# Performance work log

Measured on AMD Instinct MI355X. Metric: run time of the kernel, lower is better.

## Reference

```python
import jax, jax.numpy as jnp
import numpy as np

SEQ = 2048
HID = 4096
N_HEADS = 32
N_KV = 8
HEAD_DIM = 128
EPS = 1e-6


def _rope_tables(max_pos, dim, base=10000.0):
    inv_freq = 1.0 / (base ** (np.arange(0, dim, 2, dtype=np.float32) / dim))
    t = np.arange(max_pos, dtype=np.float32)
    freqs = np.outer(t, inv_freq)                     # [P, D/2]
    emb = np.concatenate([freqs, freqs], axis=-1)     # [P, D]
    return jnp.asarray(np.cos(emb)), jnp.asarray(np.sin(emb))


def setup_inputs() -> dict:
    key = jax.random.key(0)
    ks = jax.random.split(key, 6)
    s = 0.02
    cos, sin = _rope_tables(SEQ, HEAD_DIM)
    causal = jnp.tril(jnp.ones((SEQ, SEQ), dtype=bool))
    attn_mask = jnp.where(causal, 0.0, -1e9).astype(jnp.float32)
    return {
        "x": jax.random.normal(ks[0], (SEQ, HID), dtype=jnp.float32),
        "position_ids": jnp.arange(SEQ, dtype=jnp.int32),
        "cos": cos,
        "sin": sin,
        "attn_mask": attn_mask,
        "Wq": jax.random.normal(ks[1], (HID, N_HEADS * HEAD_DIM), dtype=jnp.float32) * s,
        "Wk": jax.random.normal(ks[2], (HID, N_KV * HEAD_DIM), dtype=jnp.float32) * s,
        "Wv": jax.random.normal(ks[3], (HID, N_KV * HEAD_DIM), dtype=jnp.float32) * s,
        "Wo": jax.random.normal(ks[4], (N_HEADS * HEAD_DIM, HID), dtype=jnp.float32) * s,
        "q_norm_w": jnp.ones((HEAD_DIM,), dtype=jnp.float32),
        "k_norm_w": jnp.ones((HEAD_DIM,), dtype=jnp.float32),
    }


def _rms_norm(x, w):
    # x: [H, S, D]; normalize over last dim
    return w * (x * jax.lax.rsqrt(jnp.mean(x * x, axis=-1, keepdims=True) + EPS))


def _apply_rope(x, cos, sin, position_ids):
    # x: [H, S, D]; cos/sin: [P, D]
    c = cos[position_ids][None]  # [1, S, D]
    s = sin[position_ids][None]
    half = x.shape[-1] // 2
    x1, x2 = x[..., :half], x[..., half:]
    rotated = jnp.concatenate([-x2, x1], axis=-1)
    return x * c + rotated * s


def reference(x, position_ids, cos, sin, attn_mask, Wq, Wk, Wv, Wo, q_norm_w, k_norm_w):
    S = x.shape[0]
    q = (x @ Wq).reshape(S, N_HEADS, HEAD_DIM).transpose(1, 0, 2)   # [H, S, D]
    k = (x @ Wk).reshape(S, N_KV, HEAD_DIM).transpose(1, 0, 2)      # [Hkv, S, D]
    v = (x @ Wv).reshape(S, N_KV, HEAD_DIM).transpose(1, 0, 2)
    q = _rms_norm(q, q_norm_w)
    k = _rms_norm(k, k_norm_w)
    q = _apply_rope(q, cos, sin, position_ids)
    k = _apply_rope(k, cos, sin, position_ids)
    # GQA: repeat_interleave kv heads to match q heads
    groups = N_HEADS // N_KV
    k = jnp.repeat(k, groups, axis=0)  # [H, S, D]
    v = jnp.repeat(v, groups, axis=0)
    scores = jnp.einsum("hqd,hkd->hqk", q, k) * (HEAD_DIM ** -0.5)
    scores = scores + attn_mask  # broadcast [S,S] -> [H,S,S]
    attn = jax.nn.softmax(scores.astype(jnp.float32), axis=-1).astype(x.dtype)
    out = jnp.einsum("hqk,hkd->hqd", attn, v)   # [H, S, D]
    out = out.transpose(1, 0, 2).reshape(S, N_HEADS * HEAD_DIM)
    return out @ Wo
```

## Files before the change

### kernel.cpp

```cpp
#include <hip/hip_runtime.h>

typedef unsigned short u16;
typedef __attribute__((ext_vector_type(8))) short bf16x8;
typedef __attribute__((ext_vector_type(4))) float f32x4;

__device__ __forceinline__ float bf2f(u16 b) {
    unsigned int u = ((unsigned int)b) << 16;
    float f;
    __builtin_memcpy(&f, &u, 4);
    return f;
}
__device__ __forceinline__ u16 f2bf(float f) {
    unsigned int u;
    __builtin_memcpy(&u, &f, 4);
    unsigned int r = u + 0x7FFFu + ((u >> 16) & 1u);
    return (u16)(r >> 16);
}

__device__ __forceinline__ void async_copy16(const void* g, void* lds) {
    __builtin_amdgcn_global_load_lds(
        (const __attribute__((address_space(1))) unsigned int*)g,
        (__attribute__((address_space(3))) unsigned int*)lds, 16, 0, 0);
}

#define MFMA(a, b, c) __builtin_amdgcn_mfma_f32_16x16x32_bf16((a), (b), (c), 0, 0, 0)

__global__ __launch_bounds__(256) void cvt_f32_bf16(
    const float* __restrict__ src, u16* __restrict__ dst)
{
    int i = (blockIdx.x * 256 + threadIdx.x) * 8;
    float4 a = *(const float4*)(src + i);
    float4 b = *(const float4*)(src + i + 4);
    uint4 o;
    u16* po = (u16*)&o;
    po[0] = f2bf(a.x); po[1] = f2bf(a.y); po[2] = f2bf(a.z); po[3] = f2bf(a.w);
    po[4] = f2bf(b.x); po[5] = f2bf(b.y); po[6] = f2bf(b.z); po[7] = f2bf(b.w);
    *(uint4*)(dst + i) = o;
}

__global__ __launch_bounds__(256) void transpose_cvt(
    const float* __restrict__ src, u16* __restrict__ dst, int R, int C)
{
    __shared__ u16 T[64][65];
    int r0 = blockIdx.y * 64, c0 = blockIdx.x * 64;
    int t = threadIdx.x;
#pragma unroll
    for (int i = 0; i < 4; ++i) {
        int c = i * 256 + t;
        int row = c >> 4, col4 = (c & 15) * 4;
        float4 v = *(const float4*)(src + (size_t)(r0 + row) * C + c0 + col4);
        T[row][col4 + 0] = f2bf(v.x);
        T[row][col4 + 1] = f2bf(v.y);
        T[row][col4 + 2] = f2bf(v.z);
        T[row][col4 + 3] = f2bf(v.w);
    }
    __syncthreads();
#pragma unroll
    for (int i = 0; i < 2; ++i) {
        int c = i * 256 + t;
        int row = c >> 3, col8 = (c & 7) * 8;
        uint4 o;
        u16* po = (u16*)&o;
#pragma unroll
        for (int j = 0; j < 8; ++j) po[j] = T[col8 + j][row];
        *(uint4*)(dst + (size_t)(c0 + row) * R + r0 + col8) = o;
    }
}

template <bool F32OUT>
__global__ __launch_bounds__(256) void gemm_bt(
    const u16* __restrict__ A, const u16* __restrict__ Bt, void* __restrict__ Cp,
    int M, int N, int K)
{
    __shared__ u16 As[128][64];
    __shared__ u16 Bs[128][64];
    int tid = threadIdx.x;
    int w = tid >> 6, lane = tid & 63;
    int quad = lane >> 4, l15 = lane & 15;
    int m0 = blockIdx.y * 128, n0 = blockIdx.x * 128;
    int wm = w >> 1, wn = w & 1;

    f32x4 acc[4][4] = {};

    for (int k0 = 0; k0 < K; k0 += 64) {
#pragma unroll
        for (int i = 0; i < 4; ++i) {
            int row = w * 32 + i * 8 + (lane >> 3);
            int s = lane & 7;
            int gc = s ^ (row & 7);
            async_copy16(A + (size_t)(m0 + row) * K + k0 + gc * 8, &As[w * 32 + i * 8][0]);
            async_copy16(Bt + (size_t)(n0 + row) * K + k0 + gc * 8, &Bs[w * 32 + i * 8][0]);
        }
        __syncthreads();
#pragma unroll
        for (int kk = 0; kk < 2; ++kk) {
            bf16x8 a[4], b[4];
            int kq = kk * 4 + quad;
#pragma unroll
            for (int mt = 0; mt < 4; ++mt) {
                int m = wm * 64 + mt * 16 + l15;
                a[mt] = *(const bf16x8*)&As[m][(kq ^ (m & 7)) * 8];
            }
#pragma unroll
            for (int nt = 0; nt < 4; ++nt) {
                int n = wn * 64 + nt * 16 + l15;
                b[nt] = *(const bf16x8*)&Bs[n][(kq ^ (n & 7)) * 8];
            }
#pragma unroll
            for (int mt = 0; mt < 4; ++mt)
#pragma unroll
                for (int nt = 0; nt < 4; ++nt)
                    acc[mt][nt] = MFMA(a[mt], b[nt], acc[mt][nt]);
        }
        __syncthreads();
    }

#pragma unroll
    for (int mt = 0; mt < 4; ++mt)
#pragma unroll
        for (int nt = 0; nt < 4; ++nt)
#pragma unroll
            for (int r = 0; r < 4; ++r) {
                int m = m0 + wm * 64 + mt * 16 + quad * 4 + r;
                int n = n0 + wn * 64 + nt * 16 + l15;
                if (F32OUT)
                    ((float*)Cp)[(size_t)m * N + n] = acc[mt][nt][r];
                else
                    ((u16*)Cp)[(size_t)m * N + n] = f2bf(acc[mt][nt][r]);
            }
}

__global__ __launch_bounds__(256) void norm_rope(
    const u16* __restrict__ QKV, const int* __restrict__ pos,
    const float* __restrict__ cosT, const float* __restrict__ sinT,
    const float* __restrict__ qw, const float* __restrict__ kw,
    u16* __restrict__ Qr, u16* __restrict__ Kr)
{
    int gw = blockIdx.x * 4 + (threadIdx.x >> 6);
    int lane = threadIdx.x & 63;
    int s = gw / 40;
    int hh = gw - s * 40;
    bool isq = hh < 32;
    int h = isq ? hh : hh - 32;
    int col0 = isq ? h * 128 : 4096 + h * 128;
    const u16* x = QKV + (size_t)s * 6144 + col0;
    float x1 = bf2f(x[lane]);
    float x2 = bf2f(x[lane + 64]);
    float ss = x1 * x1 + x2 * x2;
#pragma unroll
    for (int m = 1; m < 64; m <<= 1) ss += __shfl_xor(ss, m);
    float r = rsqrtf(ss * (1.0f / 128.0f) + 1e-6f);
    const float* wgt = isq ? qw : kw;
    float y1 = x1 * r * wgt[lane];
    float y2 = x2 * r * wgt[lane + 64];
    int p = pos[s];
    float c1 = cosT[p * 128 + lane], c2 = cosT[p * 128 + lane + 64];
    float s1 = sinT[p * 128 + lane], s2 = sinT[p * 128 + lane + 64];
    float o1 = y1 * c1 - y2 * s1;
    float o2 = y2 * c2 + y1 * s2;
    u16* dst = (isq ? Qr : Kr) + ((size_t)h * 2048 + s) * 128;
    dst[lane] = f2bf(o1);
    dst[lane + 64] = f2bf(o2);
}

__global__ __launch_bounds__(256) void v_transpose(
    const u16* __restrict__ QKV, u16* __restrict__ Vt)
{
    __shared__ u16 T[64][130];
    int s0 = blockIdx.x * 64;
    int kh = blockIdx.y;
    int t = threadIdx.x;
#pragma unroll
    for (int i = 0; i < 4; ++i) {
        int c = i * 256 + t;
        int srow = c >> 4, d8 = (c & 15) * 8;
        uint4 v = *(const uint4*)(QKV + (size_t)(s0 + srow) * 6144 + 5120 + kh * 128 + d8);
        const u16* pv = (const u16*)&v;
#pragma unroll
        for (int j = 0; j < 8; ++j) T[srow][d8 + j] = pv[j];
    }
    __syncthreads();
#pragma unroll
    for (int i = 0; i < 4; ++i) {
        int c = i * 256 + t;
        int drow = c >> 3, s8 = (c & 7) * 8;
        uint4 o;
        u16* po = (u16*)&o;
#pragma unroll
        for (int j = 0; j < 8; ++j) po[j] = T[s8 + j][drow];
        *(uint4*)(Vt + ((size_t)kh * 128 + drow) * 2048 + s0 + s8) = o;
    }
}

__global__ __launch_bounds__(256, 2) void flash_attn2(
    const u16* __restrict__ Qr, const u16* __restrict__ Kr,
    const u16* __restrict__ Vt, u16* __restrict__ O)
{
    __shared__ u16 Ks[2][64][128];
    __shared__ u16 Vs[2][128][64];
    __shared__ u16 Ps[4][32][64];

    int f = blockIdx.x + 64 * blockIdx.y;
    int lo = f & 255, hi = f >> 8;
    int qt  = hi ? 63 - (lo & 63) : (lo & 63);
    int kvh = (lo >> 6) + hi * 4;

    int tid = threadIdx.x;
    int w = tid >> 6, lane = tid & 63;
    int quad = lane >> 4, l15 = lane & 15;
    int h = kvh * 4 + w;
    int q0 = qt * 32;
    int nkt = qt / 2 + 1;

    bf16x8 qf[2][4];
#pragma unroll
    for (int mt = 0; mt < 2; ++mt) {
        const u16* qb = Qr + ((size_t)h * 2048 + q0 + mt * 16 + l15) * 128;
#pragma unroll
        for (int kk = 0; kk < 4; ++kk)
            qf[mt][kk] = *(const bf16x8*)(qb + kk * 32 + quad * 8);
    }

    float m_i[8], l_i[8];
#pragma unroll
    for (int r = 0; r < 8; ++r) { m_i[r] = -__builtin_inff(); l_i[r] = 0.0f; }
    f32x4 acc[2][8] = {};

    const float scale = 0.08838834764831845f;
    const float L2E = 1.44269504f;

    auto stage = [&](int kt, int b) {
        int k0 = kt * 64;
#pragma unroll
        for (int i = 0; i < 4; ++i) {
            int idx = (w * 4 + i) * 64 + lane;
            int krow = idx >> 4, kp = idx & 15;
            int kg = (kp & 8) | ((kp ^ krow) & 7);
            async_copy16(Kr + ((size_t)kvh * 2048 + k0 + krow) * 128 + kg * 8,
                         &Ks[b][(w * 4 + i) * 4][0]);
            int vrow = idx >> 3, vp = idx & 7;
            int vg = vp ^ (vrow & 7);
            async_copy16(Vt + ((size_t)kvh * 128 + vrow) * 2048 + k0 + vg * 8,
                         &Vs[b][(w * 4 + i) * 8][0]);
        }
    };

    stage(0, 0);

    for (int kt = 0; kt < nkt; ++kt) {
        int b = kt & 1;
        int k0 = kt * 64;
        __syncthreads();
        if (kt + 1 < nkt) stage(kt + 1, b ^ 1);

        f32x4 sa[2][4] = {};
#pragma unroll
        for (int nt = 0; nt < 4; ++nt) {
            int krow = nt * 16 + l15;
#pragma unroll
            for (int kk = 0; kk < 4; ++kk) {
                int kq = kk * 4 + quad;
                int kph = (kq & 8) | ((kq ^ krow) & 7);
                bf16x8 kf = *(const bf16x8*)&Ks[b][krow][kph * 8];
                sa[0][nt] = MFMA(qf[0][kk], kf, sa[0][nt]);
                sa[1][nt] = MFMA(qf[1][kk], kf, sa[1][nt]);
            }
        }

        bool last = (kt == nkt - 1);
        float pv[2][4][4], mloc[8];
#pragma unroll
        for (int r = 0; r < 8; ++r) mloc[r] = -__builtin_inff();
#pragma unroll
        for (int mt = 0; mt < 2; ++mt)
#pragma unroll
            for (int nt = 0; nt < 4; ++nt)
#pragma unroll
                for (int r = 0; r < 4; ++r) {
                    float v = sa[mt][nt][r] * scale;
                    if (last) {
                        int key = k0 + nt * 16 + l15;
                        int qrow = q0 + mt * 16 + quad * 4 + r;
                        if (key > qrow) v = -__builtin_inff();
                    }
                    pv[mt][nt][r] = v;
                    mloc[mt * 4 + r] = fmaxf(mloc[mt * 4 + r], v);
                }
#pragma unroll
        for (int r = 0; r < 8; ++r)
#pragma unroll
            for (int m = 1; m < 16; m <<= 1)
                mloc[r] = fmaxf(mloc[r], __shfl_xor(mloc[r], m));

        float alpha[8];
#pragma unroll
        for (int mt = 0; mt < 2; ++mt)
#pragma unroll
            for (int r = 0; r < 4; ++r) {
                int rr = mt * 4 + r;
                float mnew = fmaxf(m_i[rr], mloc[rr]);
                alpha[rr] = exp2f((m_i[rr] - mnew) * L2E);
                m_i[rr] = mnew;
                float rs = 0.0f;
#pragma unroll
                for (int nt = 0; nt < 4; ++nt) {
                    float p = exp2f((pv[mt][nt][r] - mnew) * L2E);
                    pv[mt][nt][r] = p;
                    rs += p;
                }
#pragma unroll
                for (int m = 1; m < 16; m <<= 1) rs += __shfl_xor(rs, m);
                l_i[rr] = l_i[rr] * alpha[rr] + rs;
            }
#pragma unroll
        for (int mt = 0; mt < 2; ++mt)
#pragma unroll
            for (int nt = 0; nt < 8; ++nt)
#pragma unroll
                for (int r = 0; r < 4; ++r) acc[mt][nt][r] *= alpha[mt * 4 + r];

#pragma unroll
        for (int mt = 0; mt < 2; ++mt)
#pragma unroll
            for (int nt = 0; nt < 4; ++nt)
#pragma unroll
                for (int r = 0; r < 4; ++r) {
                    int row = mt * 16 + quad * 4 + r;
                    int col = nt * 16 + l15;
                    int ph = ((col >> 3) ^ (row & 7)) * 8 + (col & 7);
                    Ps[w][row][ph] = f2bf(pv[mt][nt][r]);
                }
        asm volatile("s_waitcnt lgkmcnt(0)" ::: "memory");

        bf16x8 pf[2][2];
#pragma unroll
        for (int mt = 0; mt < 2; ++mt) {
            int row = mt * 16 + l15;
#pragma unroll
            for (int kk = 0; kk < 2; ++kk)
                pf[mt][kk] = *(const bf16x8*)&Ps[w][row][((kk * 4 + quad) ^ (row & 7)) * 8];
        }

#pragma unroll
        for (int nt = 0; nt < 8; ++nt) {
            int vrow = nt * 16 + l15;
#pragma unroll
            for (int kk = 0; kk < 2; ++kk) {
                int vph = (kk * 4 + quad) ^ (vrow & 7);
                bf16x8 vf = *(const bf16x8*)&Vs[b][vrow][vph * 8];
                acc[0][nt] = MFMA(pf[0][kk], vf, acc[0][nt]);
                acc[1][nt] = MFMA(pf[1][kk], vf, acc[1][nt]);
            }
        }
    }

#pragma unroll
    for (int mt = 0; mt < 2; ++mt)
#pragma unroll
        for (int nt = 0; nt < 8; ++nt)
#pragma unroll
            for (int r = 0; r < 4; ++r) {
                int qrow = q0 + mt * 16 + quad * 4 + r;
                int d = nt * 16 + l15;
                O[(size_t)qrow * 4096 + h * 128 + d] =
                    f2bf(acc[mt][nt][r] / l_i[mt * 4 + r]);
            }
}

extern "C" void kernel_launch(void* const* d_in, const int* in_sizes, int n_in,
                              void* d_out, int out_size, void* d_ws, size_t ws_size,
                              hipStream_t stream) {
    const float* x    = (const float*)d_in[0];
    const int*   pos  = (const int*)d_in[1];
    const float* cosT = (const float*)d_in[2];
    const float* sinT = (const float*)d_in[3];
    const float* Wq = (const float*)d_in[5];
    const float* Wk = (const float*)d_in[6];
    const float* Wv = (const float*)d_in[7];
    const float* Wo = (const float*)d_in[8];
    const float* qw = (const float*)d_in[9];
    const float* kw = (const float*)d_in[10];
    float* out = (float*)d_out;

    char* ws = (char*)d_ws;
    u16* WT  = (u16*)ws;
    u16* QKV = (u16*)(ws + 50331648ull);
    u16* Qr  = (u16*)(ws + 75497472ull);
    u16* Kr  = (u16*)(ws + 92274688ull);
    u16* Vt  = (u16*)(ws + 96468992ull);
    u16* Xb  = (u16*)(ws + 100663296ull);
    u16* AttnOut = QKV;

    dim3 blk(256);
    cvt_f32_bf16<<<dim3(4096), blk, 0, stream>>>(x, Xb);
    transpose_cvt<<<dim3(64, 64), blk, 0, stream>>>(Wq, WT, 4096, 4096);
    transpose_cvt<<<dim3(16, 64), blk, 0, stream>>>(Wk, WT + 4096ull * 4096, 4096, 1024);
    transpose_cvt<<<dim3(16, 64), blk, 0, stream>>>(Wv, WT + 5120ull * 4096, 4096, 1024);
    gemm_bt<false><<<dim3(48, 16), blk, 0, stream>>>(Xb, WT, QKV, 2048, 6144, 4096);
    norm_rope<<<dim3(20480), blk, 0, stream>>>(QKV, pos, cosT, sinT, qw, kw, Qr, Kr);
    v_transpose<<<dim3(32, 8), blk, 0, stream>>>(QKV, Vt);
    transpose_cvt<<<dim3(64, 64), blk, 0, stream>>>(Wo, WT, 4096, 4096);
    flash_attn2<<<dim3(64, 8), blk, 0, stream>>>(Qr, Kr, Vt, AttnOut);
    gemm_bt<true><<<dim3(32, 16), blk, 0, stream>>>(AttnOut, WT, out, 2048, 4096, 4096);
}
```

Before: 552.4 us.

## Drop online-softmax max tracking, split long causal rows across blocks with atomics

```diff
diff --git a/kernel.cpp b/kernel.cpp
--- a/kernel.cpp
+++ b/kernel.cpp
@@ -13,8 +13,7 @@
 __device__ __forceinline__ u16 f2bf(float f) {
     unsigned int u;
     __builtin_memcpy(&u, &f, 4);
-    unsigned int r = u + 0x7FFFu + ((u >> 16) & 1u);
-    return (u16)(r >> 16);
+    return (u16)((u + 0x8000u) >> 16);
 }
 
 __device__ __forceinline__ void async_copy16(const void* g, void* lds) {
@@ -192,25 +191,38 @@
     }
 }
 
-__global__ __launch_bounds__(256, 2) void flash_attn2(
+__global__ __launch_bounds__(256, 3) void flash_attn3(
     const u16* __restrict__ Qr, const u16* __restrict__ Kr,
-    const u16* __restrict__ Vt, u16* __restrict__ O)
-{
-    __shared__ u16 Ks[2][64][128];
-    __shared__ u16 Vs[2][128][64];
+    const u16* __restrict__ Vt, u16* __restrict__ O,
+    float* __restrict__ Oacc, float* __restrict__ Lacc)
+{
+    __shared__ u16 Ks[64][128];
+    __shared__ u16 Vs[128][64];
     __shared__ u16 Ps[4][32][64];
 
-    int f = blockIdx.x + 64 * blockIdx.y;
-    int lo = f & 255, hi = f >> 8;
-    int qt  = hi ? 63 - (lo & 63) : (lo & 63);
-    int kvh = (lo >> 6) + hi * 4;
+    int f = blockIdx.x;
+    int kvh = f / 95;
+    int j = f - kvh * 95;
+    int qt, kt0, len;
+    bool split;
+    if (j < 33) {
+        qt = j; kt0 = 0; len = (qt >> 1) + 1; split = false;
+    } else {
+        int jj = j - 33;
+        qt = 33 + (jj >> 1);
+        int n = (qt >> 1) + 1;
+        int h1 = (n + 1) >> 1;
+        if (jj & 1) { kt0 = h1; len = n - h1; }
+        else        { kt0 = 0;  len = h1; }
+        split = true;
+    }
+    int ndiag = qt >> 1;
+    int q0 = qt * 32;
 
     int tid = threadIdx.x;
     int w = tid >> 6, lane = tid & 63;
     int quad = lane >> 4, l15 = lane & 15;
     int h = kvh * 4 + w;
-    int q0 = qt * 32;
-    int nkt = qt / 2 + 1;
 
     bf16x8 qf[2][4];
 #pragma unroll
@@ -221,37 +233,31 @@
             qf[mt][kk] = *(const bf16x8*)(qb + kk * 32 + quad * 8);
     }
 
-    float m_i[8], l_i[8];
-#pragma unroll
-    for (int r = 0; r < 8; ++r) { m_i[r] = -__builtin_inff(); l_i[r] = 0.0f; }
     f32x4 acc[2][8] = {};
-
-    const float scale = 0.08838834764831845f;
-    const float L2E = 1.44269504f;
-
-    auto stage = [&](int kt, int b) {
+    f32x4 accl[2] = {};
+    bf16x8 ones;
+#pragma unroll
+    for (int i = 0; i < 8; ++i) ones[i] = (short)0x3F80;
+
+    const float C = 0.08838834764831845f * 1.44269504f;
+
+    for (int it = 0; it < len; ++it) {
+        int kt = kt0 + it;
         int k0 = kt * 64;
+        __syncthreads();
 #pragma unroll
         for (int i = 0; i < 4; ++i) {
             int idx = (w * 4 + i) * 64 + lane;
             int krow = idx >> 4, kp = idx & 15;
             int kg = (kp & 8) | ((kp ^ krow) & 7);
             async_copy16(Kr + ((size_t)kvh * 2048 + k0 + krow) * 128 + kg * 8,
-                         &Ks[b][(w * 4 + i) * 4][0]);
+                         &Ks[(w * 4 + i) * 4][0]);
             int vrow = idx >> 3, vp = idx & 7;
             int vg = vp ^ (vrow & 7);
             async_copy16(Vt + ((size_t)kvh * 128 + vrow) * 2048 + k0 + vg * 8,
-                         &Vs[b][(w * 4 + i) * 8][0]);
-        }
-    };
-
-    stage(0, 0);
-
-    for (int kt = 0; kt < nkt; ++kt) {
-        int b = kt & 1;
-        int k0 = kt * 64;
+                         &Vs[(w * 4 + i) * 8][0]);
+        }
         __syncthreads();
-        if (kt + 1 < nkt) stage(kt + 1, b ^ 1);
 
         f32x4 sa[2][4] = {};
 #pragma unroll
@@ -261,74 +267,29 @@
             for (int kk = 0; kk < 4; ++kk) {
                 int kq = kk * 4 + quad;
                 int kph = (kq & 8) | ((kq ^ krow) & 7);
-                bf16x8 kf = *(const bf16x8*)&Ks[b][krow][kph * 8];
+                bf16x8 kf = *(const bf16x8*)&Ks[krow][kph * 8];
                 sa[0][nt] = MFMA(qf[0][kk], kf, sa[0][nt]);
                 sa[1][nt] = MFMA(qf[1][kk], kf, sa[1][nt]);
             }
         }
 
-        bool last = (kt == nkt - 1);
-        float pv[2][4][4], mloc[8];
-#pragma unroll
-        for (int r = 0; r < 8; ++r) mloc[r] = -__builtin_inff();
+        bool diag = (kt == ndiag);
 #pragma unroll
         for (int mt = 0; mt < 2; ++mt)
 #pragma unroll
             for (int nt = 0; nt < 4; ++nt)
 #pragma unroll
                 for (int r = 0; r < 4; ++r) {
-                    float v = sa[mt][nt][r] * scale;
-                    if (last) {
+                    float p = exp2f(sa[mt][nt][r] * C);
+                    if (diag) {
                         int key = k0 + nt * 16 + l15;
                         int qrow = q0 + mt * 16 + quad * 4 + r;
-                        if (key > qrow) v = -__builtin_inff();
+                        if (key > qrow) p = 0.0f;
                     }
-                    pv[mt][nt][r] = v;
-                    mloc[mt * 4 + r] = fmaxf(mloc[mt * 4 + r], v);
-                }
-#pragma unroll
-        for (int r = 0; r < 8; ++r)
-#pragma unroll
-            for (int m = 1; m < 16; m <<= 1)
-                mloc[r] = fmaxf(mloc[r], __shfl_xor(mloc[r], m));
-
-        float alpha[8];
-#pragma unroll
-        for (int mt = 0; mt < 2; ++mt)
-#pragma unroll
-            for (int r = 0; r < 4; ++r) {
-                int rr = mt * 4 + r;
-                float mnew = fmaxf(m_i[rr], mloc[rr]);
-                alpha[rr] = exp2f((m_i[rr] - mnew) * L2E);
-                m_i[rr] = mnew;
-                float rs = 0.0f;
-#pragma unroll
-                for (int nt = 0; nt < 4; ++nt) {
-                    float p = exp2f((pv[mt][nt][r] - mnew) * L2E);
-                    pv[mt][nt][r] = p;
-                    rs += p;
-                }
-#pragma unroll
-                for (int m = 1; m < 16; m <<= 1) rs += __shfl_xor(rs, m);
-                l_i[rr] = l_i[rr] * alpha[rr] + rs;
-            }
-#pragma unroll
-        for (int mt = 0; mt < 2; ++mt)
-#pragma unroll
-            for (int nt = 0; nt < 8; ++nt)
-#pragma unroll
-                for (int r = 0; r < 4; ++r) acc[mt][nt][r] *= alpha[mt * 4 + r];
-
-#pragma unroll
-        for (int mt = 0; mt < 2; ++mt)
-#pragma unroll
-            for (int nt = 0; nt < 4; ++nt)
-#pragma unroll
-                for (int r = 0; r < 4; ++r) {
                     int row = mt * 16 + quad * 4 + r;
                     int col = nt * 16 + l15;
                     int ph = ((col >> 3) ^ (row & 7)) * 8 + (col & 7);
-                    Ps[w][row][ph] = f2bf(pv[mt][nt][r]);
+                    Ps[w][row][ph] = f2bf(p);
                 }
         asm volatile("s_waitcnt lgkmcnt(0)" ::: "memory");
 
@@ -347,24 +308,63 @@
 #pragma unroll
             for (int kk = 0; kk < 2; ++kk) {
                 int vph = (kk * 4 + quad) ^ (vrow & 7);
-                bf16x8 vf = *(const bf16x8*)&Vs[b][vrow][vph * 8];
+                bf16x8 vf = *(const bf16x8*)&Vs[vrow][vph * 8];
                 acc[0][nt] = MFMA(pf[0][kk], vf, acc[0][nt]);
                 acc[1][nt] = MFMA(pf[1][kk], vf, acc[1][nt]);
             }
         }
-    }
-
-#pragma unroll
-    for (int mt = 0; mt < 2; ++mt)
-#pragma unroll
-        for (int nt = 0; nt < 8; ++nt)
-#pragma unroll
-            for (int r = 0; r < 4; ++r) {
-                int qrow = q0 + mt * 16 + quad * 4 + r;
-                int d = nt * 16 + l15;
-                O[(size_t)qrow * 4096 + h * 128 + d] =
-                    f2bf(acc[mt][nt][r] / l_i[mt * 4 + r]);
-            }
+#pragma unroll
+        for (int mt = 0; mt < 2; ++mt)
+#pragma unroll
+            for (int kk = 0; kk < 2; ++kk)
+                accl[mt] = MFMA(pf[mt][kk], ones, accl[mt]);
+    }
+
+    if (!split) {
+#pragma unroll
+        for (int mt = 0; mt < 2; ++mt)
+#pragma unroll
+            for (int nt = 0; nt < 8; ++nt)
+#pragma unroll
+                for (int r = 0; r < 4; ++r) {
+                    int qrow = q0 + mt * 16 + quad * 4 + r;
+                    int d = nt * 16 + l15;
+                    O[(size_t)qrow * 4096 + h * 128 + d] =
+                        f2bf(acc[mt][nt][r] / accl[mt][r]);
+                }
+    } else {
+        int base = q0 - 1056;
+#pragma unroll
+        for (int mt = 0; mt < 2; ++mt)
+#pragma unroll
+            for (int nt = 0; nt < 8; ++nt)
+#pragma unroll
+                for (int r = 0; r < 4; ++r) {
+                    int row = base + mt * 16 + quad * 4 + r;
+                    int d = nt * 16 + l15;
+                    atomicAdd(&Oacc[((size_t)h * 992 + row) * 128 + d], acc[mt][nt][r]);
+                }
+        if (l15 == 0) {
+#pragma unroll
+            for (int mt = 0; mt < 2; ++mt)
+#pragma unroll
+                for (int r = 0; r < 4; ++r)
+                    atomicAdd(&Lacc[h * 992 + base + mt * 16 + quad * 4 + r],
+                              accl[mt][r]);
+        }
+    }
+}
+
+__global__ __launch_bounds__(256) void normalize_split(
+    const float* __restrict__ Oacc, const float* __restrict__ Lacc,
+    u16* __restrict__ O)
+{
+    int e = blockIdx.x * 256 + threadIdx.x;
+    int hd = e / 126976;
+    int rem = e - hd * 126976;
+    int row = rem >> 7, d = rem & 127;
+    float v = Oacc[e] / Lacc[hd * 992 + row];
+    O[(size_t)(1056 + row) * 4096 + hd * 128 + d] = f2bf(v);
 }
 
 extern "C" void kernel_launch(void* const* d_in, const int* in_sizes, int n_in,
@@ -390,6 +390,8 @@
     u16* Vt  = (u16*)(ws + 96468992ull);
     u16* Xb  = (u16*)(ws + 100663296ull);
     u16* AttnOut = QKV;
+    float* Oacc = (float*)Xb;
+    float* Lacc = (float*)((char*)Xb + 16252928ull);
 
     dim3 blk(256);
     cvt_f32_bf16<<<dim3(4096), blk, 0, stream>>>(x, Xb);
@@ -397,9 +399,11 @@
     transpose_cvt<<<dim3(16, 64), blk, 0, stream>>>(Wk, WT + 4096ull * 4096, 4096, 1024);
     transpose_cvt<<<dim3(16, 64), blk, 0, stream>>>(Wv, WT + 5120ull * 4096, 4096, 1024);
     gemm_bt<false><<<dim3(48, 16), blk, 0, stream>>>(Xb, WT, QKV, 2048, 6144, 4096);
+    hipMemsetAsync(Oacc, 0, 16379904ull, stream);
     norm_rope<<<dim3(20480), blk, 0, stream>>>(QKV, pos, cosT, sinT, qw, kw, Qr, Kr);
     v_transpose<<<dim3(32, 8), blk, 0, stream>>>(QKV, Vt);
     transpose_cvt<<<dim3(64, 64), blk, 0, stream>>>(Wo, WT, 4096, 4096);
-    flash_attn2<<<dim3(64, 8), blk, 0, stream>>>(Qr, Kr, Vt, AttnOut);
+    flash_attn3<<<dim3(760), blk, 0, stream>>>(Qr, Kr, Vt, AttnOut, Oacc, Lacc);
+    normalize_split<<<dim3(15872), blk, 0, stream>>>(Oacc, Lacc, AttnOut);
     gemm_bt<true><<<dim3(32, 16), blk, 0, stream>>>(AttnOut, WT, out, 2048, 4096, 4096);
 }
```

Result: slower. 660.3 us (+19.5%).
